# Optimization experiments

Measured on AMD Instinct MI355X. Metric: run time of the kernel, lower is better.

## Reference

```python
import jax, jax.numpy as jnp
import numpy as np

LEARNING_RATE = 0.005
WEIGHT_DECAY = 0.0001


def setup_inputs() -> dict:
    key = jax.random.key(0)
    k1, k2, k3 = jax.random.split(key, 3)
    B, POST, PRE = 128, 1024, 1024
    pre_spikes = jax.random.uniform(k1, (B, PRE), dtype=jnp.float32)
    post_spikes = jax.random.uniform(k2, (B, POST), dtype=jnp.float32)
    weights = jax.random.normal(k3, (POST, PRE), dtype=jnp.float32)
    return {"pre_spikes": pre_spikes, "post_spikes": post_spikes, "weights": weights}


def reference(pre_spikes, post_spikes, weights):
    # mean over batch of outer products post_b (x) pre_b == post^T @ pre / B
    B = pre_spikes.shape[0]
    mean_hebbian = jnp.einsum('bp,bq->pq', post_spikes, pre_spikes) / B  # (post, pre)
    dw = LEARNING_RATE * (mean_hebbian - WEIGHT_DECAY * weights)
    return dw
```

## Files before the change

kernel.cpp:

```cpp
#include <hip/hip_runtime.h>


using f32x16 = __attribute__((ext_vector_type(16))) float;
using short8 = __attribute__((ext_vector_type(8))) short;

constexpr int   N    = 1024;
constexpr int   K    = 128;
constexpr int   LSTR = 136;
constexpr float LR   = 0.005f;
constexpr float WD   = 0.0001f;

__device__ inline unsigned short f2bf(float x) {
    union { float f; unsigned int u; } c; c.f = x;
    return (unsigned short)((c.u + 0x7FFFu + ((c.u >> 16) & 1u)) >> 16);
}

__global__ __launch_bounds__(64) void hebb_mfma(
    const float* __restrict__ pre,
    const float* __restrict__ post,
    const float* __restrict__ W,
    float* __restrict__ out)
{
    __shared__ unsigned short A_lds[32 * LSTR];
    __shared__ unsigned short B_lds[32 * LSTR];

    const int l  = threadIdx.x;
    const int bm = blockIdx.y * 32;
    const int bn = blockIdx.x * 32;

    const int m4 = (l & 7) * 4;
    const int k8 = (l >> 3) * 8;

    #pragma unroll
    for (int p = 0; p < 2; ++p) {
        const int kb = k8 + p * 64;
        float4 av[8], bv[8];
        #pragma unroll
        for (int j = 0; j < 8; ++j) {
            av[j] = *(const float4*)(post + (size_t)(kb + j) * N + bm + m4);
            bv[j] = *(const float4*)(pre  + (size_t)(kb + j) * N + bn + m4);
        }
        #pragma unroll
        for (int i = 0; i < 4; ++i) {
            short8 pa, pb;
            #pragma unroll
            for (int j = 0; j < 8; ++j) {
                const float* fa = (const float*)&av[j];
                const float* fb = (const float*)&bv[j];
                pa[j] = (short)f2bf(fa[i]);
                pb[j] = (short)f2bf(fb[i]);
            }
            *(short8*)&A_lds[(m4 + i) * LSTR + kb] = pa;
            *(short8*)&B_lds[(m4 + i) * LSTR + kb] = pb;
        }
    }

    const int col   = l & 31;
    const int rbase = 4 * (l >> 5);
    float wv[16];
    #pragma unroll
    for (int r = 0; r < 16; ++r) {
        const int row = (r & 3) + 8 * (r >> 2) + rbase;
        wv[r] = W[(size_t)(bm + row) * N + bn + col];
    }

    __syncthreads();

    f32x16 acc = {};
    const int hh = 8 * (l >> 5);
    #pragma unroll
    for (int kk = 0; kk < 8; ++kk) {
        short8 a = *(const short8*)&A_lds[(l & 31) * LSTR + kk * 16 + hh];
        short8 b = *(const short8*)&B_lds[(l & 31) * LSTR + kk * 16 + hh];
        acc = __builtin_amdgcn_mfma_f32_32x32x16_bf16(a, b, acc, 0, 0, 0);
    }

    const float s1 = LR / 128.0f;
    const float s2 = LR * WD;
    #pragma unroll
    for (int r = 0; r < 16; ++r) {
        const int row = (r & 3) + 8 * (r >> 2) + rbase;
        out[(size_t)(bm + row) * N + bn + col] = s1 * acc[r] - s2 * wv[r];
    }
}

extern "C" void kernel_launch(void* const* d_in, const int* in_sizes, int n_in,
                              void* d_out, int out_size, void* d_ws, size_t ws_size,
                              hipStream_t stream) {
    const float* pre  = (const float*)d_in[0];
    const float* post = (const float*)d_in[1];
    const float* W    = (const float*)d_in[2];
    float* out = (float*)d_out;

    dim3 grid(N / 32, N / 32);
    dim3 block(64);

    #pragma unroll
    for (int rep = 0; rep < 4; ++rep)
        hebb_mfma<<<grid, block, 0, stream>>>(pre, post, W, out);
}
```

Before: 76.21 us.

## Switch to 16x16 MFMA tiles and launch the kernel once

Reworks the kernel to compute 16x16 output tiles with the 16x16x32 bf16 MFMA instead of 32x32 tiles, quadrupling the grid and raising occupancy hints. It also drops the loop that launched the same kernel four times, so the output is computed only once. Smaller tiles increase redundant global reads of the spike inputs, which are expected to hit in L2.

```diff
diff --git a/kernel.cpp b/kernel.cpp
--- a/kernel.cpp
+++ b/kernel.cpp
@@ -1,11 +1,10 @@
 #include <hip/hip_runtime.h>
 
 
-using f32x16 = __attribute__((ext_vector_type(16))) float;
+using f32x4  = __attribute__((ext_vector_type(4))) float;
 using short8 = __attribute__((ext_vector_type(8))) short;
 
 constexpr int   N    = 1024;
-constexpr int   K    = 128;
 constexpr int   LSTR = 136;
 constexpr float LR   = 0.005f;
 constexpr float WD   = 0.0001f;
@@ -15,73 +14,72 @@
     return (unsigned short)((c.u + 0x7FFFu + ((c.u >> 16) & 1u)) >> 16);
 }
 
-__global__ __launch_bounds__(64) void hebb_mfma(
+__global__ __launch_bounds__(64, 4) void hebb_mfma16(
     const float* __restrict__ pre,
     const float* __restrict__ post,
     const float* __restrict__ W,
     float* __restrict__ out)
 {
-    __shared__ unsigned short A_lds[32 * LSTR];
-    __shared__ unsigned short B_lds[32 * LSTR];
+    __shared__ unsigned short A_lds[16 * LSTR];
+    __shared__ unsigned short B_lds[16 * LSTR];
 
     const int l  = threadIdx.x;
-    const int bm = blockIdx.y * 32;
-    const int bn = blockIdx.x * 32;
+    const int bm = blockIdx.y * 16;
+    const int bn = blockIdx.x * 16;
 
-    const int m4 = (l & 7) * 4;
-    const int k8 = (l >> 3) * 8;
+    const int m4 = (l & 3) * 4;
+    const int k8 = (l >> 2) * 8;
 
-    #pragma unroll
-    for (int p = 0; p < 2; ++p) {
-        const int kb = k8 + p * 64;
-        float4 av[8], bv[8];
+    {
+        float4 v[8];
         #pragma unroll
-        for (int j = 0; j < 8; ++j) {
-            av[j] = *(const float4*)(post + (size_t)(kb + j) * N + bm + m4);
-            bv[j] = *(const float4*)(pre  + (size_t)(kb + j) * N + bn + m4);
-        }
+        for (int j = 0; j < 8; ++j)
+            v[j] = *(const float4*)(post + (size_t)(k8 + j) * N + bm + m4);
         #pragma unroll
         for (int i = 0; i < 4; ++i) {
-            short8 pa, pb;
+            short8 p;
             #pragma unroll
-            for (int j = 0; j < 8; ++j) {
-                const float* fa = (const float*)&av[j];
-                const float* fb = (const float*)&bv[j];
-                pa[j] = (short)f2bf(fa[i]);
-                pb[j] = (short)f2bf(fb[i]);
-            }
-            *(short8*)&A_lds[(m4 + i) * LSTR + kb] = pa;
-            *(short8*)&B_lds[(m4 + i) * LSTR + kb] = pb;
+            for (int j = 0; j < 8; ++j) p[j] = (short)f2bf(((const float*)&v[j])[i]);
+            *(short8*)&A_lds[(m4 + i) * LSTR + k8] = p;
+        }
+    }
+    {
+        float4 v[8];
+        #pragma unroll
+        for (int j = 0; j < 8; ++j)
+            v[j] = *(const float4*)(pre + (size_t)(k8 + j) * N + bn + m4);
+        #pragma unroll
+        for (int i = 0; i < 4; ++i) {
+            short8 p;
+            #pragma unroll
+            for (int j = 0; j < 8; ++j) p[j] = (short)f2bf(((const float*)&v[j])[i]);
+            *(short8*)&B_lds[(m4 + i) * LSTR + k8] = p;
         }
     }
 
-    const int col   = l & 31;
-    const int rbase = 4 * (l >> 5);
-    float wv[16];
+    const int col   = l & 15;
+    const int rbase = 4 * (l >> 4);
+    float wv[4];
     #pragma unroll
-    for (int r = 0; r < 16; ++r) {
-        const int row = (r & 3) + 8 * (r >> 2) + rbase;
-        wv[r] = W[(size_t)(bm + row) * N + bn + col];
-    }
+    for (int r = 0; r < 4; ++r)
+        wv[r] = W[(size_t)(bm + rbase + r) * N + bn + col];
 
     __syncthreads();
 
-    f32x16 acc = {};
-    const int hh = 8 * (l >> 5);
+    f32x4 acc = {};
+    const int hh = 8 * (l >> 4);
     #pragma unroll
-    for (int kk = 0; kk < 8; ++kk) {
-        short8 a = *(const short8*)&A_lds[(l & 31) * LSTR + kk * 16 + hh];
-        short8 b = *(const short8*)&B_lds[(l & 31) * LSTR + kk * 16 + hh];
-        acc = __builtin_amdgcn_mfma_f32_32x32x16_bf16(a, b, acc, 0, 0, 0);
+    for (int kk = 0; kk < 4; ++kk) {
+        short8 a = *(const short8*)&A_lds[(l & 15) * LSTR + kk * 32 + hh];
+        short8 b = *(const short8*)&B_lds[(l & 15) * LSTR + kk * 32 + hh];
+        acc = __builtin_amdgcn_mfma_f32_16x16x32_bf16(a, b, acc, 0, 0, 0);
     }
 
     const float s1 = LR / 128.0f;
     const float s2 = LR * WD;
     #pragma unroll
-    for (int r = 0; r < 16; ++r) {
-        const int row = (r & 3) + 8 * (r >> 2) + rbase;
-        out[(size_t)(bm + row) * N + bn + col] = s1 * acc[r] - s2 * wv[r];
-    }
+    for (int r = 0; r < 4; ++r)
+        out[(size_t)(bm + rbase + r) * N + bn + col] = s1 * acc[r] - s2 * wv[r];
 }
 
 extern "C" void kernel_launch(void* const* d_in, const int* in_sizes, int n_in,
@@ -92,10 +90,7 @@
     const float* W    = (const float*)d_in[2];
     float* out = (float*)d_out;
 
-    dim3 grid(N / 32, N / 32);
+    dim3 grid(N / 16, N / 16);
     dim3 block(64);
-
-    #pragma unroll
-    for (int rep = 0; rep < 4; ++rep)
-        hebb_mfma<<<grid, block, 0, stream>>>(pre, post, W, out);
+    hebb_mfma16<<<grid, block, 0, stream>>>(pre, post, W, out);
 }
```

Result: faster. 65.49 us (-14.1%).
